# Kernel tuning notes

Measured on AMD Instinct MI355X. Metric: run time of the kernel, lower is better.

Reference implementation:

```python
import jax, jax.numpy as jnp
import numpy as np

EPS = 1e-5
SLOPE = 0.2  # LeakyReLU negative slope


def _leaky(x):
    return jnp.where(x > 0, x, SLOPE * x)


def _bn(x, gamma, beta, axes):
    # training-mode batchnorm: biased variance over `axes`, channel axis kept
    mean = jnp.mean(x, axis=axes, keepdims=True)
    var = jnp.var(x, axis=axes, keepdims=True)
    return (x - mean) * jax.lax.rsqrt(var + EPS) * gamma + beta


def setup_inputs() -> dict:
    key = jax.random.key(0)
    ks = jax.random.split(key, 8)
    T, B, C, H, W, TXT = 33, 256, 512, 4, 4, 256
    std = 0.02  # normal init per weights_init
    return {
        "frames": jax.random.normal(ks[0], (T, B, C, H, W), jnp.float32),
        "sent": jax.random.normal(ks[1], (B, TXT), jnp.float32),
        # sent_map: Linear(TXT, TXT) + BN1d
        "W_lin": jax.random.normal(ks[2], (TXT, TXT), jnp.float32) * std,
        "b_lin": jnp.zeros((TXT,), jnp.float32),
        "g_bn_s": 1.0 + jax.random.normal(ks[3], (TXT,), jnp.float32) * std,
        "b_bn_s": jnp.zeros((TXT,), jnp.float32),
        # motion_map: Conv2d(512,512,1,bias=False) + BN2d
        "W_mm": jax.random.normal(ks[4], (C, C), jnp.float32) * std,
        "g_bn_m": 1.0 + jax.random.normal(ks[5], (C,), jnp.float32) * std,
        "b_bn_m": jnp.zeros((C,), jnp.float32),
        # predictor conv1: Conv2d(512+256, 512, 1, bias=False) + BN2d
        "W_p1": jax.random.normal(ks[6], (C, C + TXT), jnp.float32) * std,
        "g_bn_p": 1.0 + jax.random.normal(ks[7], (C,), jnp.float32) * std,
        "b_bn_p": jnp.zeros((C,), jnp.float32),
        # predictor conv2: Conv2d(512, 1, 4, 2, 0, bias=False); 4x4 input -> 1x1 out
        "W_p2": jax.random.normal(jax.random.fold_in(key, 99), (C, H, W), jnp.float32) * std,
    }


def reference(frames, sent, W_lin, b_lin, g_bn_s, b_bn_s,
              W_mm, g_bn_m, b_bn_m, W_p1, g_bn_p, b_bn_p, W_p2):
    # sent_map: Linear + BN1d(batch stats) + LeakyReLU
    s = sent @ W_lin.T + b_lin                      # [B, TXT]
    s = _leaky(_bn(s, g_bn_s, b_bn_s, axes=(0,)))   # [B, TXT]

    # frame differences: [T-1, B, C, H, W]
    motions = frames[1:] - frames[:-1]

    # motion_map 1x1 conv (no bias) + per-frame BN2d + LeakyReLU
    m = jnp.einsum('tbchw,oc->tbohw', motions, W_mm)
    g = g_bn_m[None, None, :, None, None]
    b = b_bn_m[None, None, :, None, None]
    m = _leaky(_bn(m, g, b, axes=(1, 3, 4)))        # BN stats per frame t, over (B,H,W)

    # broadcast sentence vector over spatial dims (replaces nested python loops)
    T, B, _, H, W = m.shape
    s_dupe = jnp.broadcast_to(s[None, :, :, None, None], (T, B, s.shape[1], H, W))
    ms = jnp.concatenate([m, s_dupe], axis=2)       # [T, B, 768, H, W]

    # predictor: 1x1 conv + per-frame BN2d + LeakyReLU
    p = jnp.einsum('tbchw,oc->tbohw', ms, W_p1)
    gp = g_bn_p[None, None, :, None, None]
    bp = b_bn_p[None, None, :, None, None]
    p = _leaky(_bn(p, gp, bp, axes=(1, 3, 4)))

    # 4x4 stride-2 valid conv on 4x4 input == full contraction -> [T, B]
    out = jax.nn.sigmoid(jnp.einsum('tbchw,chw->tb', p, W_p2))
    return out
```

## Files before the change

### kernel.cpp

```cpp
#include <hip/hip_runtime.h>
#include <hip/hip_bf16.h>

typedef __attribute__((ext_vector_type(8))) unsigned short ushort8;
typedef __attribute__((ext_vector_type(8))) short bf16x8;
typedef __attribute__((ext_vector_type(4))) float f32x4;

#define TM 32
#define NB 256
#define NC 512
#define NO 512
#define HW 16
#define TXT 256

#define SB()     __builtin_amdgcn_sched_barrier(0)
#define BAR()    __builtin_amdgcn_s_barrier()
#define WAITV2() asm volatile("s_waitcnt vmcnt(2) lgkmcnt(0)" ::: "memory")
#define WAITV0() asm volatile("s_waitcnt vmcnt(0) lgkmcnt(0)" ::: "memory")
#define WAITL()  asm volatile("s_waitcnt lgkmcnt(0)" ::: "memory")

__device__ __forceinline__ float bf2f(unsigned short u) {
    return __uint_as_float(((unsigned)u) << 16);
}
__device__ __forceinline__ unsigned pk2bf(float lo, float hi) {
    __hip_bfloat162 h = __float22bfloat162_rn(float2{lo, hi});
    return *reinterpret_cast<unsigned*>(&h);
}
__device__ __forceinline__ float leaky_f(float x) { return fmaxf(x, 0.2f * x); }

__device__ __forceinline__ void gl_lds16(const void* g, void* l) {
    __builtin_amdgcn_global_load_lds(
        (const __attribute__((address_space(1))) unsigned int*)g,
        (__attribute__((address_space(3))) unsigned int*)l, 16, 0, 0);
}

__global__ __launch_bounds__(256)
void kprep_w(const float* __restrict__ Wmm, const float* __restrict__ Wp1,
             const float* __restrict__ Wp2,
             unsigned short* __restrict__ WmmBf, unsigned short* __restrict__ Wp1Bf,
             float* __restrict__ Wp2T)
{
    const int bid = blockIdx.x, tid = threadIdx.x;
    if (bid < 512) {
        const float2 v = *reinterpret_cast<const float2*>(Wmm + (size_t)bid * 512 + tid * 2);
        ((unsigned*)WmmBf)[bid * 256 + tid] = pk2bf(v.x, v.y);
    } else if (bid < 1024) {
        const int o = bid - 512;
        const float2 v = *reinterpret_cast<const float2*>(Wp1 + (size_t)o * 768 + tid * 2);
        ((unsigned*)Wp1Bf)[o * 256 + tid] = pk2bf(v.x, v.y);
    } else {
        const int i = (bid - 1024) * 256 + tid;
        const int hw = i >> 9, o = i & 511;
        Wp2T[i] = Wp2[o * 16 + hw];
    }
}

__global__ __launch_bounds__(256)
void kprep_diff(const float* __restrict__ frames, unsigned short* __restrict__ mdT)
{
    __shared__ __attribute__((aligned(16))) char lds[16 * 1040];
    const int bx = blockIdx.x;
    const int tg = bx >> 8, b = bx & 255;
    const int t0 = tg * 4;
    const int tid = threadIdx.x;
    const int cb  = (tid >> 2) * 2;
    const int hw0 = (tid & 3) * 4;
    const int hw  = tid >> 4, cg = tid & 15;
    const float* fb = frames + (size_t)t0 * 2097152 + (size_t)b * 8192;

    float4 pA[4], pB[4], cA[4], cB[4];
    #pragma unroll
    for (int it = 0; it < 4; ++it) {
        const int c = cb + it * 128;
        pA[it] = *reinterpret_cast<const float4*>(fb + c * 16 + hw0);
        pB[it] = *reinterpret_cast<const float4*>(fb + (c + 1) * 16 + hw0);
    }
    #pragma unroll
    for (int dt = 0; dt < 4; ++dt) {
        const float* fc = fb + (size_t)(dt + 1) * 2097152;
        #pragma unroll
        for (int it = 0; it < 4; ++it) {
            const int c = cb + it * 128;
            cA[it] = *reinterpret_cast<const float4*>(fc + c * 16 + hw0);
            cB[it] = *reinterpret_cast<const float4*>(fc + (c + 1) * 16 + hw0);
        }
        #pragma unroll
        for (int it = 0; it < 4; ++it) {
            const int c = cb + it * 128;
            float dA[4], dB[4];
            dA[0] = cA[it].x - pA[it].x; dA[1] = cA[it].y - pA[it].y;
            dA[2] = cA[it].z - pA[it].z; dA[3] = cA[it].w - pA[it].w;
            dB[0] = cB[it].x - pB[it].x; dB[1] = cB[it].y - pB[it].y;
            dB[2] = cB[it].z - pB[it].z; dB[3] = cB[it].w - pB[it].w;
            #pragma unroll
            for (int j = 0; j < 4; ++j)
                *reinterpret_cast<unsigned*>(lds + (hw0 + j) * 1040 + c * 2) = pk2bf(dA[j], dB[j]);
        }
        __syncthreads();
        unsigned short* outp = mdT + ((size_t)((t0 + dt) * 4096 + b * 16 + hw)) * 512;
        #pragma unroll
        for (int r = 0; r < 4; ++r) {
            const int c16 = cg + r * 16;
            const uint4 v = *reinterpret_cast<const uint4*>(lds + hw * 1040 + c16 * 16);
            *reinterpret_cast<uint4*>(outp + c16 * 8) = v;
        }
        __syncthreads();
        #pragma unroll
        for (int it = 0; it < 4; ++it) { pA[it] = cA[it]; pB[it] = cB[it]; }
    }
}

__global__ __launch_bounds__(256)
void k1_sent(const float* __restrict__ sent, const float* __restrict__ W_lin,
             const float* __restrict__ b_lin, const float* __restrict__ g_bn_s,
             const float* __restrict__ b_bn_s, float* __restrict__ s_t)
{
    const int j = blockIdx.x;
    const int b = threadIdx.x;
    __shared__ float wl[TXT];
    wl[b] = W_lin[j * TXT + b];
    __syncthreads();
    float acc = b_lin[j];
    const float* srow = sent + b * TXT;
    #pragma unroll 4
    for (int k = 0; k < TXT; k += 4) {
        float4 sv = *reinterpret_cast<const float4*>(srow + k);
        acc = fmaf(sv.x, wl[k], acc);
        acc = fmaf(sv.y, wl[k+1], acc);
        acc = fmaf(sv.z, wl[k+2], acc);
        acc = fmaf(sv.w, wl[k+3], acc);
    }
    float s1 = acc, s2 = acc * acc;
    #pragma unroll
    for (int m = 1; m < 64; m <<= 1) { s1 += __shfl_xor(s1, m, 64); s2 += __shfl_xor(s2, m, 64); }
    __shared__ float r1[4], r2[4];
    if ((b & 63) == 0) { r1[b >> 6] = s1; r2[b >> 6] = s2; }
    __syncthreads();
    const float invN = 1.0f / 256.0f;
    float mean = (r1[0] + r1[1] + r1[2] + r1[3]) * invN;
    float var  = (r2[0] + r2[1] + r2[2] + r2[3]) * invN - mean * mean;
    float rstd = rsqrtf(var + 1e-5f);
    float y = (acc - mean) * rstd * g_bn_s[j] + b_bn_s[j];
    s_t[j * NB + b] = leaky_f(y);
}

__global__ __launch_bounds__(256)
void k2_sp(const float* __restrict__ s_t, const float* __restrict__ W_p1,
           float* __restrict__ sp_bt)
{
    const int o = blockIdx.x;
    const int b = threadIdx.x;
    __shared__ float wl[TXT];
    wl[b] = W_p1[o * (NC + TXT) + NC + b];
    __syncthreads();
    float acc = 0.0f;
    #pragma unroll 8
    for (int k = 0; k < TXT; ++k)
        acc = fmaf(s_t[k * NB + b], wl[k], acc);
    sp_bt[(size_t)b * NO + o] = acc;
}


__global__ __launch_bounds__(256, 4)
void k3_mfma(const unsigned short* __restrict__ WmmBf, const unsigned short* __restrict__ mdT,
             unsigned short* __restrict__ mraw,
             float* __restrict__ ssum, float* __restrict__ ssq)
{
    __shared__ __attribute__((aligned(16))) char smem[32768];
    const int bx0 = blockIdx.x;
    const int bx = (bx0 & 7) * 512 + (bx0 >> 3);
    const int ot = bx & 3, nt = (bx >> 2) & 31, t = bx >> 7;
    const int o0 = ot * 128, n0 = nt * 128;
    const int tid = threadIdx.x;
    const int w = tid >> 6, l = tid & 63;
    const int wo = w >> 1, wn = w & 1;
    const int l15 = l & 15, l16 = l >> 4;

    const char* Ag = (const char*)WmmBf + (size_t)o0 * 1024;

    int srcOffA[2], dstOffA[2];
    #pragma unroll
    for (int i = 0; i < 2; ++i) {
        const int rb = (w << 5) + (i << 4);
        const int row = rb + (l >> 2);
        srcOffA[i] = row * 1024 + (((l & 3) ^ ((row >> 1) & 3)) << 4);
        dstOffA[i] = rb * 64;
    }

    const int rowB_s = tid >> 1, h = tid & 1;
    const char* mrow = (const char*)mdT + ((size_t)(t * 4096 + n0 + rowB_s)) * 1024 + h * 32;
    const int bbase = 8192 + rowB_s * 64;
    const int bswz = (rowB_s >> 1) & 3;

    int offA[4], offB[4];
    #pragma unroll
    for (int m = 0; m < 4; ++m) {
        const int rowA = wo * 64 + m * 16 + l15;
        const int rowB = wn * 64 + m * 16 + l15;
        offA[m] = rowA * 64 + ((l16 ^ ((rowA >> 1) & 3)) << 4);
        offB[m] = 8192 + rowB * 64 + ((l16 ^ ((rowB >> 1) & 3)) << 4);
    }

    f32x4 acc[4][4];
    #pragma unroll
    for (int i = 0; i < 4; ++i)
        #pragma unroll
        for (int j = 0; j < 4; ++j) acc[i][j] = (f32x4)0.0f;

    ushort8 u0[2], u1[2];

    auto writeB = [&](const ushort8* uu, int dstbase) {
        #pragma unroll
        for (int q = 0; q < 2; ++q)
            *reinterpret_cast<uint4*>(smem + dstbase + bbase + ((((h << 1) + q) ^ bswz) << 4)) =
                *reinterpret_cast<const uint4*>(&uu[q]);
    };

    #pragma unroll
    for (int q = 0; q < 2; ++q) u0[q] = *reinterpret_cast<const ushort8*>(mrow + q * 16);
    #pragma unroll
    for (int i = 0; i < 2; ++i) gl_lds16(Ag + srcOffA[i], smem + dstOffA[i]);
    SB();
    writeB(u0, 0);
    #pragma unroll
    for (int q = 0; q < 2; ++q) u1[q] = *reinterpret_cast<const ushort8*>(mrow + 64 + q * 16);
    SB(); WAITV2(); SB(); BAR();

    #pragma unroll
    for (int kc = 0; kc < 16; ++kc) {
        const int cur = (kc & 1) << 14;
        const int nxt = 16384 - cur;
        if (kc < 15) {
            #pragma unroll
            for (int i = 0; i < 2; ++i)
                gl_lds16(Ag + srcOffA[i] + (kc + 1) * 64, smem + nxt + dstOffA[i]);
            SB();
            if ((kc & 1) == 0) {
                writeB(u1, nxt);
                if (kc < 14) {
                    #pragma unroll
                    for (int q = 0; q < 2; ++q)
                        u0[q] = *reinterpret_cast<const ushort8*>(mrow + (kc + 2) * 64 + q * 16);
                }
            } else {
                writeB(u0, nxt);
                if (kc < 14) {
                    #pragma unroll
                    for (int q = 0; q < 2; ++q)
                        u1[q] = *reinterpret_cast<const ushort8*>(mrow + (kc + 2) * 64 + q * 16);
                }
            }
            SB();
        }
        {
            bf16x8 a[4], b[4];
            #pragma unroll
            for (int m = 0; m < 4; ++m) a[m] = *reinterpret_cast<const bf16x8*>(smem + cur + offA[m]);
            #pragma unroll
            for (int n = 0; n < 4; ++n) b[n] = *reinterpret_cast<const bf16x8*>(smem + cur + offB[n]);
            #pragma unroll
            for (int m = 0; m < 4; ++m)
                #pragma unroll
                for (int n = 0; n < 4; ++n)
                    acc[m][n] = __builtin_amdgcn_mfma_f32_16x16x32_bf16(a[m], b[n], acc[m][n], 0, 0, 0);
        }
        SB();
        if (kc < 14)       { WAITV2(); }
        else if (kc == 14) { WAITV0(); }
        else               { WAITL();  }
        SB();
        BAR();
    }

    #pragma unroll
    for (int m = 0; m < 4; ++m) {
        #pragma unroll
        for (int r = 0; r < 4; ++r) {
            float s1 = 0.0f, s2 = 0.0f;
            #pragma unroll
            for (int nn = 0; nn < 4; ++nn) {
                const float v = acc[m][nn][r];
                s1 += v; s2 = fmaf(v, v, s2);
            }
            #pragma unroll
            for (int msk = 1; msk < 16; msk <<= 1) {
                s1 += __shfl_xor(s1, msk, 64);
                s2 += __shfl_xor(s2, msk, 64);
            }
            if (l15 == 0) {
                const int o = o0 + wo * 64 + m * 16 + (l16 << 2) + r;
                atomicAdd(&ssum[t * NO + o], s1);
                atomicAdd(&ssq[t * NO + o], s2);
            }
        }
    }

    char* ep = smem;
    #pragma unroll
    for (int m = 0; m < 4; ++m) {
        #pragma unroll
        for (int nn = 0; nn < 4; ++nn) {
            uint2 u;
            u.x = pk2bf(acc[m][nn][0], acc[m][nn][1]);
            u.y = pk2bf(acc[m][nn][2], acc[m][nn][3]);
            const int row = wn * 64 + nn * 16 + l15;
            const int g   = wo * 8 + m * 2 + (l16 >> 1);
            const int off = row * 256 + ((g ^ (row & 7)) << 4) + ((l16 & 1) << 3);
            *reinterpret_cast<uint2*>(ep + off) = u;
        }
    }
    SB(); WAITL(); SB(); BAR();
    #pragma unroll
    for (int p = 0; p < 8; ++p) {
        const int row = (p << 4) + (tid >> 4);
        const int c   = tid & 15;
        const uint4 v = *reinterpret_cast<const uint4*>(ep + row * 256 + ((c ^ (row & 7)) << 4));
        *reinterpret_cast<uint4*>((char*)mraw + ((size_t)(t * 4096 + n0 + row)) * 1024
                                  + o0 * 2 + (c << 4)) = v;
    }
}

__global__ __launch_bounds__(256)
void kstats(const float* __restrict__ ssum, const float* __restrict__ ssq,
            const float* __restrict__ g, const float* __restrict__ bb,
            float* __restrict__ alpha, float* __restrict__ beta)
{
    const int i = blockIdx.x * 256 + threadIdx.x;
    const int o = i & 511;
    const float invN = 1.0f / 4096.0f;
    float mean = ssum[i] * invN;
    float var  = ssq[i] * invN - mean * mean;
    float rstd = rsqrtf(var + 1e-5f);
    float a = rstd * g[o];
    alpha[i] = a;
    beta[i]  = fmaf(-mean, a, bb[o]);
}

__global__ __launch_bounds__(256, 4)
void k5_mfma(const unsigned short* __restrict__ Wp1Bf, const unsigned short* __restrict__ mraw,
             const float* __restrict__ am, const float* __restrict__ bm,
             const float* __restrict__ sp_bt,
             unsigned short* __restrict__ praw,
             float* __restrict__ ssum, float* __restrict__ ssq)
{
    __shared__ __attribute__((aligned(16))) char smem[36864];
    float* alf = (float*)(smem + 32768);
    float* bet = (float*)(smem + 34816);
    const int bx0 = blockIdx.x;
    const int bx = (bx0 & 7) * 512 + (bx0 >> 3);
    const int ot = bx & 3, nt = (bx >> 2) & 31, t = bx >> 7;
    const int o0 = ot * 128, n0 = nt * 128;
    const int tid = threadIdx.x;
    const int w = tid >> 6, l = tid & 63;
    const int wo = w >> 1, wn = w & 1;
    const int l15 = l & 15, l16 = l >> 4;

    const char* Ag = (const char*)Wp1Bf + (size_t)o0 * 1024;

    int srcOffA[2], dstOffA[2];
    #pragma unroll
    for (int i = 0; i < 2; ++i) {
        const int rb = (w << 5) + (i << 4);
        const int row = rb + (l >> 2);
        srcOffA[i] = row * 1024 + (((l & 3) ^ ((row >> 1) & 3)) << 4);
        dstOffA[i] = rb * 64;
    }

    const int rowB_s = tid >> 1, h = tid & 1;
    const char* mrow = (const char*)mraw + ((size_t)(t * 4096 + n0 + rowB_s)) * 1024 + h * 32;
    const int bbase = 8192 + rowB_s * 64;
    const int bswz = (rowB_s >> 1) & 3;

    int offA[4], offB[4];
    #pragma unroll
    for (int m = 0; m < 4; ++m) {
        const int rowA = wo * 64 + m * 16 + l15;
        const int rowB = wn * 64 + m * 16 + l15;
        offA[m] = rowA * 64 + ((l16 ^ ((rowA >> 1) & 3)) << 4);
        offB[m] = 8192 + rowB * 64 + ((l16 ^ ((rowB >> 1) & 3)) << 4);
    }

    f32x4 acc[4][4];
    #pragma unroll
    for (int i = 0; i < 4; ++i)
        #pragma unroll
        for (int j = 0; j < 4; ++j) acc[i][j] = (f32x4)0.0f;

    ushort8 u0[2], u1[2];

    auto procB = [&](const ushort8* uu, int kc, int dstbase) {
        #pragma unroll
        for (int q = 0; q < 2; ++q) {
            const int kbase = kc * 32 + h * 16 + q * 8;
            float v[8];
            #pragma unroll
            for (int e = 0; e < 8; ++e)
                v[e] = leaky_f(fmaf(bf2f(uu[q][e]), alf[kbase + e], bet[kbase + e]));
            uint4 pk;
            pk.x = pk2bf(v[0], v[1]);
            pk.y = pk2bf(v[2], v[3]);
            pk.z = pk2bf(v[4], v[5]);
            pk.w = pk2bf(v[6], v[7]);
            *reinterpret_cast<uint4*>(smem + dstbase + bbase + ((((h << 1) + q) ^ bswz) << 4)) = pk;
        }
    };

    {
        const float* amt = am + t * NC;
        const float* bmt = bm + t * NC;
        const float2 a2 = *reinterpret_cast<const float2*>(amt + tid * 2);
        const float2 b2 = *reinterpret_cast<const float2*>(bmt + tid * 2);
        *reinterpret_cast<float2*>(alf + tid * 2) = a2;
        *reinterpret_cast<float2*>(bet + tid * 2) = b2;
    }
    #pragma unroll
    for (int q = 0; q < 2; ++q) u0[q] = *reinterpret_cast<const ushort8*>(mrow + q * 16);
    #pragma unroll
    for (int i = 0; i < 2; ++i) gl_lds16(Ag + srcOffA[i], smem + dstOffA[i]);
    SB(); WAITL(); SB(); BAR();
    procB(u0, 0, 0);
    #pragma unroll
    for (int q = 0; q < 2; ++q) u1[q] = *reinterpret_cast<const ushort8*>(mrow + 64 + q * 16);
    SB(); WAITV2(); SB(); BAR();

    #pragma unroll
    for (int kc = 0; kc < 16; ++kc) {
        const int cur = (kc & 1) << 14;
        const int nxt = 16384 - cur;
        if (kc < 15) {
            #pragma unroll
            for (int i = 0; i < 2; ++i)
                gl_lds16(Ag + srcOffA[i] + (kc + 1) * 64, smem + nxt + dstOffA[i]);
            SB();
            if ((kc & 1) == 0) {
                procB(u1, kc + 1, nxt);
                if (kc < 14) {
                    #pragma unroll
                    for (int q = 0; q < 2; ++q)
                        u0[q] = *reinterpret_cast<const ushort8*>(mrow + (kc + 2) * 64 + q * 16);
                }
            } else {
                procB(u0, kc + 1, nxt);
                if (kc < 14) {
                    #pragma unroll
                    for (int q = 0; q < 2; ++q)
                        u1[q] = *reinterpret_cast<const ushort8*>(mrow + (kc + 2) * 64 + q * 16);
                }
            }
            SB();
        }
        {
            bf16x8 a[4], b[4];
            #pragma unroll
            for (int m = 0; m < 4; ++m) a[m] = *reinterpret_cast<const bf16x8*>(smem + cur + offA[m]);
            #pragma unroll
            for (int n = 0; n < 4; ++n) b[n] = *reinterpret_cast<const bf16x8*>(smem + cur + offB[n]);
            #pragma unroll
            for (int m = 0; m < 4; ++m)
                #pragma unroll
                for (int n = 0; n < 4; ++n)
                    acc[m][n] = __builtin_amdgcn_mfma_f32_16x16x32_bf16(a[m], b[n], acc[m][n], 0, 0, 0);
        }
        SB();
        if (kc < 14)       { WAITV2(); }
        else if (kc == 14) { WAITV0(); }
        else               { WAITL();  }
        SB();
        BAR();
    }

    char* ep = smem;
    #pragma unroll
    for (int m = 0; m < 4; ++m) {
        const int oc = o0 + wo * 64 + m * 16 + (l16 << 2);
        float s1[4] = {0,0,0,0}, s2[4] = {0,0,0,0};
        #pragma unroll
        for (int nn = 0; nn < 4; ++nn) {
            const int b = (n0 >> 4) + wn * 4 + nn;
            const float4 sp4 = *reinterpret_cast<const float4*>(sp_bt + (size_t)b * NO + oc);
            const float spv[4] = {sp4.x, sp4.y, sp4.z, sp4.w};
            float pv[4];
            #pragma unroll
            for (int r = 0; r < 4; ++r) {
                const float v = acc[m][nn][r] + spv[r];
                pv[r] = v;
                s1[r] += v; s2[r] = fmaf(v, v, s2[r]);
            }
            uint2 uu;
            uu.x = pk2bf(pv[0], pv[1]);
            uu.y = pk2bf(pv[2], pv[3]);
            const int row = wn * 64 + nn * 16 + l15;
            const int g   = wo * 8 + m * 2 + (l16 >> 1);
            const int off = row * 256 + ((g ^ (row & 7)) << 4) + ((l16 & 1) << 3);
            *reinterpret_cast<uint2*>(ep + off) = uu;
        }
        #pragma unroll
        for (int r = 0; r < 4; ++r) {
            #pragma unroll
            for (int msk = 1; msk < 16; msk <<= 1) {
                s1[r] += __shfl_xor(s1[r], msk, 64);
                s2[r] += __shfl_xor(s2[r], msk, 64);
            }
            if (l15 == 0) {
                atomicAdd(&ssum[t * NO + oc + r], s1[r]);
                atomicAdd(&ssq[t * NO + oc + r], s2[r]);
            }
        }
    }
    SB(); WAITL(); SB(); BAR();
    #pragma unroll
    for (int p = 0; p < 8; ++p) {
        const int row = (p << 4) + (tid >> 4);
        const int c   = tid & 15;
        const uint4 v = *reinterpret_cast<const uint4*>(ep + row * 256 + ((c ^ (row & 7)) << 4));
        *reinterpret_cast<uint4*>((char*)praw + ((size_t)(t * 4096 + n0 + row)) * 1024
                                  + o0 * 2 + (c << 4)) = v;
    }
}

__global__ __launch_bounds__(256)
void k7_out(const unsigned short* __restrict__ praw, const float* __restrict__ ap,
            const float* __restrict__ bp, const float* __restrict__ wp2t,
            float* __restrict__ out)
{
    const int bx = blockIdx.x;
    const int t = bx >> 8, b = bx & 255;
    const int tid = threadIdx.x;
    const unsigned short* pr = praw + ((size_t)(t * 256 + b)) * 8192;
    float acc = 0.0f;
    #pragma unroll
    for (int e = 0; e < 4; ++e) {
        const int idx = e * 2048 + tid * 8;
        const int hw = idx >> 9, o = idx & 511;
        const ushort8 u = *reinterpret_cast<const ushort8*>(pr + idx);
        float av[8], bv[8], wv[8];
        *reinterpret_cast<float4*>(av)     = *reinterpret_cast<const float4*>(ap + t * NO + o);
        *reinterpret_cast<float4*>(av + 4) = *reinterpret_cast<const float4*>(ap + t * NO + o + 4);
        *reinterpret_cast<float4*>(bv)     = *reinterpret_cast<const float4*>(bp + t * NO + o);
        *reinterpret_cast<float4*>(bv + 4) = *reinterpret_cast<const float4*>(bp + t * NO + o + 4);
        *reinterpret_cast<float4*>(wv)     = *reinterpret_cast<const float4*>(wp2t + hw * NO + o);
        *reinterpret_cast<float4*>(wv + 4) = *reinterpret_cast<const float4*>(wp2t + hw * NO + o + 4);
        #pragma unroll
        for (int j = 0; j < 8; ++j) {
            const float x = leaky_f(fmaf(bf2f(u[j]), av[j], bv[j]));
            acc = fmaf(x, wv[j], acc);
        }
    }
    #pragma unroll
    for (int m = 1; m < 64; m <<= 1) acc += __shfl_xor(acc, m, 64);
    __shared__ float red[4];
    if ((tid & 63) == 0) red[tid >> 6] = acc;
    __syncthreads();
    if (tid == 0) {
        float z = red[0] + red[1] + red[2] + red[3];
        out[t * NB + b] = 1.0f / (1.0f + __expf(-z));
    }
}

extern "C" void kernel_launch(void* const* d_in, const int* in_sizes, int n_in,
                              void* d_out, int out_size, void* d_ws, size_t ws_size,
                              hipStream_t stream)
{
    const float* frames = (const float*)d_in[0];
    const float* sent   = (const float*)d_in[1];
    const float* W_lin  = (const float*)d_in[2];
    const float* b_lin  = (const float*)d_in[3];
    const float* g_bn_s = (const float*)d_in[4];
    const float* b_bn_s = (const float*)d_in[5];
    const float* W_mm   = (const float*)d_in[6];
    const float* g_bn_m = (const float*)d_in[7];
    const float* b_bn_m = (const float*)d_in[8];
    const float* W_p1   = (const float*)d_in[9];
    const float* g_bn_p = (const float*)d_in[10];
    const float* b_bn_p = (const float*)d_in[11];
    const float* W_p2   = (const float*)d_in[12];
    float* out = (float*)d_out;

    char* ws = (char*)d_ws;
    const size_t BIG = 134217728;
    unsigned short* bufA = (unsigned short*)ws;
    unsigned short* bufB = (unsigned short*)(ws + BIG);
    char* small = ws + 2 * BIG;
    float* msum = (float*)(small);
    float* msq  = (float*)(small + 65536);
    float* psum = (float*)(small + 131072);
    float* psq  = (float*)(small + 196608);
    float* am   = (float*)(small + 262144);
    float* bm   = (float*)(small + 327680);
    float* apv  = (float*)(small + 393216);
    float* bpv  = (float*)(small + 458752);
    float* s_t  = (float*)(small + 524288);
    float* sp_bt= (float*)(small + 786432);
    float* wp2t = (float*)(small + 1310720);
    unsigned short* WmmBf = (unsigned short*)(small + 1343488);
    unsigned short* Wp1Bf = (unsigned short*)(small + 1867776);

    hipMemsetAsync(small, 0, 262144, stream);
    kprep_w<<<1056, 256, 0, stream>>>(W_mm, W_p1, W_p2, WmmBf, Wp1Bf, wp2t);
    kprep_diff<<<2048, 256, 0, stream>>>(frames, bufA);
    k1_sent<<<256, 256, 0, stream>>>(sent, W_lin, b_lin, g_bn_s, b_bn_s, s_t);
    k2_sp<<<512, 256, 0, stream>>>(s_t, W_p1, sp_bt);
    k3_mfma<<<4096, 256, 0, stream>>>(WmmBf, bufA, bufB, msum, msq);
    kstats<<<64, 256, 0, stream>>>(msum, msq, g_bn_m, b_bn_m, am, bm);
    k5_mfma<<<4096, 256, 0, stream>>>(Wp1Bf, bufB, am, bm, sp_bt, bufA, psum, psq);
    kstats<<<64, 256, 0, stream>>>(psum, psq, g_bn_p, b_bn_p, apv, bpv);
    k7_out<<<8192, 256, 0, stream>>>(bufA, apv, bpv, wp2t, out);
}
```

Measured before the change: 439.3 us.

## Deepen GEMM pipelines to three stages with direct-to-LDS loads for B

In k3, B tiles are now loaded straight into LDS with global_load_lds instead of going through registers, and the LDS buffering goes from double to triple (48KB). In k5, the A tiles are triple-buffered and the raw B prefetch now looks three steps ahead, so more memory latency is hidden behind the MFMAs. The launch-bounds occupancy hint drops from 4 to 3 blocks and the vmcnt waits are reworked to match. The cost is more LDS per block, which may limit how many waves can be resident.

Result: no change. 436.6 us (-0.6%).

```diff
diff --git a/kernel.cpp b/kernel.cpp
--- a/kernel.cpp
+++ b/kernel.cpp
@@ -14,7 +14,8 @@
 
 #define SB()     __builtin_amdgcn_sched_barrier(0)
 #define BAR()    __builtin_amdgcn_s_barrier()
-#define WAITV2() asm volatile("s_waitcnt vmcnt(2) lgkmcnt(0)" ::: "memory")
+#define WAITV6() asm volatile("s_waitcnt vmcnt(6) lgkmcnt(0)" ::: "memory")
+#define WAITV4() asm volatile("s_waitcnt vmcnt(4) lgkmcnt(0)" ::: "memory")
 #define WAITV0() asm volatile("s_waitcnt vmcnt(0) lgkmcnt(0)" ::: "memory")
 #define WAITL()  asm volatile("s_waitcnt lgkmcnt(0)" ::: "memory")
 
@@ -160,12 +161,12 @@
 }
 
 
-__global__ __launch_bounds__(256, 4)
+__global__ __launch_bounds__(256, 3)
 void k3_mfma(const unsigned short* __restrict__ WmmBf, const unsigned short* __restrict__ mdT,
              unsigned short* __restrict__ mraw,
              float* __restrict__ ssum, float* __restrict__ ssq)
 {
-    __shared__ __attribute__((aligned(16))) char smem[32768];
+    __shared__ __attribute__((aligned(16))) char smem[49152];
     const int bx0 = blockIdx.x;
     const int bx = (bx0 & 7) * 512 + (bx0 >> 3);
     const int ot = bx & 3, nt = (bx >> 2) & 31, t = bx >> 7;
@@ -176,20 +177,16 @@
     const int l15 = l & 15, l16 = l >> 4;
 
     const char* Ag = (const char*)WmmBf + (size_t)o0 * 1024;
-
-    int srcOffA[2], dstOffA[2];
+    const char* Bg = (const char*)mdT + ((size_t)(t * 4096 + n0)) * 1024;
+
+    int srcOff[2], dstOff[2];
     #pragma unroll
     for (int i = 0; i < 2; ++i) {
         const int rb = (w << 5) + (i << 4);
         const int row = rb + (l >> 2);
-        srcOffA[i] = row * 1024 + (((l & 3) ^ ((row >> 1) & 3)) << 4);
-        dstOffA[i] = rb * 64;
-    }
-
-    const int rowB_s = tid >> 1, h = tid & 1;
-    const char* mrow = (const char*)mdT + ((size_t)(t * 4096 + n0 + rowB_s)) * 1024 + h * 32;
-    const int bbase = 8192 + rowB_s * 64;
-    const int bswz = (rowB_s >> 1) & 3;
+        srcOff[i] = row * 1024 + (((l & 3) ^ ((row >> 1) & 3)) << 4);
+        dstOff[i] = rb * 64;
+    }
 
     int offA[4], offB[4];
     #pragma unroll
@@ -206,51 +203,25 @@
         #pragma unroll
         for (int j = 0; j < 4; ++j) acc[i][j] = (f32x4)0.0f;
 
-    ushort8 u0[2], u1[2];
-
-    auto writeB = [&](const ushort8* uu, int dstbase) {
-        #pragma unroll
-        for (int q = 0; q < 2; ++q)
-            *reinterpret_cast<uint4*>(smem + dstbase + bbase + ((((h << 1) + q) ^ bswz) << 4)) =
-                *reinterpret_cast<const uint4*>(&uu[q]);
+    auto stage = [&](int kc, int buf) {
+        char* dst = smem + buf * 16384;
+        #pragma unroll
+        for (int i = 0; i < 2; ++i)
+            gl_lds16(Ag + srcOff[i] + kc * 64, dst + dstOff[i]);
+        #pragma unroll
+        for (int i = 0; i < 2; ++i)
+            gl_lds16(Bg + srcOff[i] + kc * 64, dst + 8192 + dstOff[i]);
     };
 
-    #pragma unroll
-    for (int q = 0; q < 2; ++q) u0[q] = *reinterpret_cast<const ushort8*>(mrow + q * 16);
-    #pragma unroll
-    for (int i = 0; i < 2; ++i) gl_lds16(Ag + srcOffA[i], smem + dstOffA[i]);
-    SB();
-    writeB(u0, 0);
-    #pragma unroll
-    for (int q = 0; q < 2; ++q) u1[q] = *reinterpret_cast<const ushort8*>(mrow + 64 + q * 16);
-    SB(); WAITV2(); SB(); BAR();
+    stage(0, 0);
+    stage(1, 1);
+    SB(); WAITV4(); SB(); BAR();
 
     #pragma unroll
     for (int kc = 0; kc < 16; ++kc) {
-        const int cur = (kc & 1) << 14;
-        const int nxt = 16384 - cur;
-        if (kc < 15) {
-            #pragma unroll
-            for (int i = 0; i < 2; ++i)
-                gl_lds16(Ag + srcOffA[i] + (kc + 1) * 64, smem + nxt + dstOffA[i]);
-            SB();
-            if ((kc & 1) == 0) {
-                writeB(u1, nxt);
-                if (kc < 14) {
-                    #pragma unroll
-                    for (int q = 0; q < 2; ++q)
-                        u0[q] = *reinterpret_cast<const ushort8*>(mrow + (kc + 2) * 64 + q * 16);
-                }
-            } else {
-                writeB(u0, nxt);
-                if (kc < 14) {
-                    #pragma unroll
-                    for (int q = 0; q < 2; ++q)
-                        u1[q] = *reinterpret_cast<const ushort8*>(mrow + (kc + 2) * 64 + q * 16);
-                }
-            }
-            SB();
-        }
+        const int cur = (kc % 3) * 16384;
+        if (kc < 14) stage(kc + 2, (kc + 2) % 3);
+        SB();
         {
             bf16x8 a[4], b[4];
             #pragma unroll
@@ -264,7 +235,7 @@
                     acc[m][n] = __builtin_amdgcn_mfma_f32_16x16x32_bf16(a[m], b[n], acc[m][n], 0, 0, 0);
         }
         SB();
-        if (kc < 14)       { WAITV2(); }
+        if (kc < 14)       { WAITV4(); }
         else if (kc == 14) { WAITV0(); }
         else               { WAITL();  }
         SB();
@@ -335,16 +306,16 @@
     beta[i]  = fmaf(-mean, a, bb[o]);
 }
 
-__global__ __launch_bounds__(256, 4)
+__global__ __launch_bounds__(256, 3)
 void k5_mfma(const unsigned short* __restrict__ Wp1Bf, const unsigned short* __restrict__ mraw,
              const float* __restrict__ am, const float* __restrict__ bm,
              const float* __restrict__ sp_bt,
              unsigned short* __restrict__ praw,
              float* __restrict__ ssum, float* __restrict__ ssq)
 {
-    __shared__ __attribute__((aligned(16))) char smem[36864];
-    float* alf = (float*)(smem + 32768);
-    float* bet = (float*)(smem + 34816);
+    __shared__ __attribute__((aligned(16))) char smem[45056];
+    float* alf = (float*)(smem + 40960);
+    float* bet = (float*)(smem + 43008);
     const int bx0 = blockIdx.x;
     const int bx = (bx0 & 7) * 512 + (bx0 >> 3);
     const int ot = bx & 3, nt = (bx >> 2) & 31, t = bx >> 7;
@@ -367,7 +338,7 @@
 
     const int rowB_s = tid >> 1, h = tid & 1;
     const char* mrow = (const char*)mraw + ((size_t)(t * 4096 + n0 + rowB_s)) * 1024 + h * 32;
-    const int bbase = 8192 + rowB_s * 64;
+    const int bbase = rowB_s * 64;
     const int bswz = (rowB_s >> 1) & 3;
 
     int offA[4], offB[4];
@@ -376,7 +347,7 @@
         const int rowA = wo * 64 + m * 16 + l15;
         const int rowB = wn * 64 + m * 16 + l15;
         offA[m] = rowA * 64 + ((l16 ^ ((rowA >> 1) & 3)) << 4);
-        offB[m] = 8192 + rowB * 64 + ((l16 ^ ((rowB >> 1) & 3)) << 4);
+        offB[m] = rowB * 64 + ((l16 ^ ((rowB >> 1) & 3)) << 4);
     }
 
     f32x4 acc[4][4];
@@ -385,22 +356,33 @@
         #pragma unroll
         for (int j = 0; j < 4; ++j) acc[i][j] = (f32x4)0.0f;
 
-    ushort8 u0[2], u1[2];
-
-    auto procB = [&](const ushort8* uu, int kc, int dstbase) {
+    ushort8 ur[3][2];
+
+    auto gldsA = [&](int kc, int buf) {
+        char* dst = smem + buf * 8192;
+        #pragma unroll
+        for (int i = 0; i < 2; ++i)
+            gl_lds16(Ag + srcOffA[i] + kc * 64, dst + dstOffA[i]);
+    };
+    auto loadU = [&](int slot, int kc) {
+        #pragma unroll
+        for (int q = 0; q < 2; ++q)
+            ur[slot][q] = *reinterpret_cast<const ushort8*>(mrow + kc * 64 + q * 16);
+    };
+    auto procB = [&](int slot, int kc, int btoff) {
         #pragma unroll
         for (int q = 0; q < 2; ++q) {
             const int kbase = kc * 32 + h * 16 + q * 8;
             float v[8];
             #pragma unroll
             for (int e = 0; e < 8; ++e)
-                v[e] = leaky_f(fmaf(bf2f(uu[q][e]), alf[kbase + e], bet[kbase + e]));
+                v[e] = leaky_f(fmaf(bf2f(ur[slot][q][e]), alf[kbase + e], bet[kbase + e]));
             uint4 pk;
             pk.x = pk2bf(v[0], v[1]);
             pk.y = pk2bf(v[2], v[3]);
             pk.z = pk2bf(v[4], v[5]);
             pk.w = pk2bf(v[6], v[7]);
-            *reinterpret_cast<uint4*>(smem + dstbase + bbase + ((((h << 1) + q) ^ bswz) << 4)) = pk;
+            *reinterpret_cast<uint4*>(smem + btoff + bbase + ((((h << 1) + q) ^ bswz) << 4)) = pk;
         }
     };
 
@@ -412,48 +394,30 @@
         *reinterpret_cast<float2*>(alf + tid * 2) = a2;
         *reinterpret_cast<float2*>(bet + tid * 2) = b2;
     }
-    #pragma unroll
-    for (int q = 0; q < 2; ++q) u0[q] = *reinterpret_cast<const ushort8*>(mrow + q * 16);
-    #pragma unroll
-    for (int i = 0; i < 2; ++i) gl_lds16(Ag + srcOffA[i], smem + dstOffA[i]);
+    loadU(0, 0);
+    gldsA(0, 0);
+    loadU(1, 1);
+    gldsA(1, 1);
+    loadU(2, 2);
     SB(); WAITL(); SB(); BAR();
-    procB(u0, 0, 0);
-    #pragma unroll
-    for (int q = 0; q < 2; ++q) u1[q] = *reinterpret_cast<const ushort8*>(mrow + 64 + q * 16);
-    SB(); WAITV2(); SB(); BAR();
+    procB(0, 0, 24576);
+    SB(); WAITV6(); SB(); BAR();
 
     #pragma unroll
     for (int kc = 0; kc < 16; ++kc) {
-        const int cur = (kc & 1) << 14;
-        const int nxt = 16384 - cur;
-        if (kc < 15) {
-            #pragma unroll
-            for (int i = 0; i < 2; ++i)
-                gl_lds16(Ag + srcOffA[i] + (kc + 1) * 64, smem + nxt + dstOffA[i]);
-            SB();
-            if ((kc & 1) == 0) {
-                procB(u1, kc + 1, nxt);
-                if (kc < 14) {
-                    #pragma unroll
-                    for (int q = 0; q < 2; ++q)
-                        u0[q] = *reinterpret_cast<const ushort8*>(mrow + (kc + 2) * 64 + q * 16);
-                }
-            } else {
-                procB(u0, kc + 1, nxt);
-                if (kc < 14) {
-                    #pragma unroll
-                    for (int q = 0; q < 2; ++q)
-                        u1[q] = *reinterpret_cast<const ushort8*>(mrow + (kc + 2) * 64 + q * 16);
-                }
-            }
-            SB();
-        }
+        const int acur = (kc % 3) * 8192;
+        const int bcur = 24576 + (kc & 1) * 8192;
+        if (kc < 14) gldsA(kc + 2, (kc + 2) % 3);
+        SB();
+        if (kc < 15) procB((kc + 1) % 3, kc + 1, 24576 + ((kc + 1) & 1) * 8192);
+        if (kc < 13) loadU(kc % 3, kc + 3);
+        SB();
         {
             bf16x8 a[4], b[4];
             #pragma unroll
-            for (int m = 0; m < 4; ++m) a[m] = *reinterpret_cast<const bf16x8*>(smem + cur + offA[m]);
-            #pragma unroll
-            for (int n = 0; n < 4; ++n) b[n] = *reinterpret_cast<const bf16x8*>(smem + cur + offB[n]);
+            for (int m = 0; m < 4; ++m) a[m] = *reinterpret_cast<const bf16x8*>(smem + acur + offA[m]);
+            #pragma unroll
+            for (int n = 0; n < 4; ++n) b[n] = *reinterpret_cast<const bf16x8*>(smem + bcur + offB[n]);
             #pragma unroll
             for (int m = 0; m < 4; ++m)
                 #pragma unroll
@@ -461,7 +425,8 @@
                     acc[m][n] = __builtin_amdgcn_mfma_f32_16x16x32_bf16(a[m], b[n], acc[m][n], 0, 0, 0);
         }
         SB();
-        if (kc < 14)       { WAITV2(); }
+        if (kc < 13)       { WAITV6(); }
+        else if (kc == 13) { WAITV4(); }
         else if (kc == 14) { WAITV0(); }
         else               { WAITL();  }
         SB();
```
